# Kernel tuning notes

Measured on AMD Instinct MI355X. Metric: run time of the kernel, lower is better.

The kernel has to match this reference:

```python
import jax, jax.numpy as jnp
import numpy as np

NEG_SLOPE = 0.2

def gat_layer(x, src, dst, W, a_src, a_dst, num_nodes):
    """PyG-style GATConv. W:[F_in,H*C], a_src/a_dst:[H,C]. Returns [N,H,C]."""
    H, C = a_src.shape
    h = (x @ W).reshape(num_nodes, H, C)                      # [N,H,C]
    e_src = jnp.sum(h * a_src, axis=-1)                       # [N,H]
    e_dst = jnp.sum(h * a_dst, axis=-1)                       # [N,H]
    e = jax.nn.leaky_relu(e_src[src] + e_dst[dst], NEG_SLOPE) # [E,H]
    # segment softmax over incoming edges of each destination node
    m = jax.ops.segment_max(e, dst, num_segments=num_nodes)
    w = jnp.exp(e - m[dst])
    z = jax.ops.segment_sum(w, dst, num_segments=num_nodes)
    alpha = w / (z[dst] + 1e-16)                               # [E,H]
    msg = h[src] * alpha[:, :, None]                           # [E,H,C]
    return jax.ops.segment_sum(msg, dst, num_segments=num_nodes)


def setup_inputs() -> dict:
    key = jax.random.key(0)
    ks = jax.random.split(key, 16)
    N, E, F_IN, HID, A, G = 50000, 800000, 128, 128, 32, 64
    x = jax.random.normal(ks[0], (N, F_IN), dtype=jnp.float32)
    edge_index = jax.random.randint(ks[1], (2, E), 0, N, dtype=jnp.int32)
    batch = jnp.sort(jax.random.randint(ks[2], (N,), 0, G, dtype=jnp.int32))
    s = 0.1
    W1 = jax.random.normal(ks[3], (F_IN, 2 * HID), jnp.float32) * s
    a_src1 = jax.random.normal(ks[4], (2, HID), jnp.float32) * s
    a_dst1 = jax.random.normal(ks[5], (2, HID), jnp.float32) * s
    b1 = jnp.zeros((2 * HID,), jnp.float32)
    W2 = jax.random.normal(ks[6], (2 * HID, HID), jnp.float32) * s
    a_src2 = jax.random.normal(ks[7], (1, HID), jnp.float32) * s
    a_dst2 = jax.random.normal(ks[8], (1, HID), jnp.float32) * s
    b2 = jnp.zeros((HID,), jnp.float32)
    Wp = jax.random.normal(ks[9], (HID, A), jnp.float32) * s
    bp = jnp.zeros((A,), jnp.float32)
    Wv = jax.random.normal(ks[10], (HID, 1), jnp.float32) * s
    bv = jnp.zeros((1,), jnp.float32)
    return {"x": x, "edge_index": edge_index, "batch": batch,
            "W1": W1, "a_src1": a_src1, "a_dst1": a_dst1, "b1": b1,
            "W2": W2, "a_src2": a_src2, "a_dst2": a_dst2, "b2": b2,
            "Wp": Wp, "bp": bp, "Wv": Wv, "bv": bv}


def reference(x, edge_index, batch, W1, a_src1, a_dst1, b1,
              W2, a_src2, a_dst2, b2, Wp, bp, Wv, bv):
    N = x.shape[0]
    G = 64  # number of graphs in the batch
    # add self-loops (PyG GATConv default)
    loop = jnp.arange(N, dtype=edge_index.dtype)
    src = jnp.concatenate([edge_index[0], loop])
    dst = jnp.concatenate([edge_index[1], loop])
    # layer 1: heads=2, concat=True
    h1 = gat_layer(x, src, dst, W1, a_src1, a_dst1, N)        # [N,2,HID]
    h1 = jax.nn.elu(h1.reshape(N, -1) + b1)                   # [N,2*HID]
    # layer 2: heads=1, concat=False (mean over heads = identity for H=1)
    h2 = gat_layer(h1, src, dst, W2, a_src2, a_dst2, N)       # [N,1,HID]
    h2 = jax.nn.elu(h2.reshape(N, -1) + b2)                   # [N,HID]
    # global mean pool over graphs
    sums = jax.ops.segment_sum(h2, batch, num_segments=G)
    cnt = jax.ops.segment_sum(jnp.ones((N,), h2.dtype), batch, num_segments=G)
    x_pool = sums / jnp.maximum(cnt, 1.0)[:, None]            # [G,HID]
    policy_logits = x_pool @ Wp + bp                          # [G,A]
    state_value = x_pool @ Wv + bv                            # [G,1]
    return (policy_logits, state_value)
```

## Files before the change

kernel.cpp:

```cpp
#include <hip/hip_runtime.h>
#include <hip/hip_bf16.h>
#include <cstdint>


typedef __attribute__((ext_vector_type(8))) short bf16x8;
typedef __attribute__((ext_vector_type(4))) float f32x4;

#define NBLK_H 160

__device__ __forceinline__ float wave_sum(float v) {
#pragma unroll
    for (int off = 32; off >= 1; off >>= 1) v += __shfl_xor(v, off, 64);
    return v;
}

__device__ __forceinline__ unsigned short f2bf(float f) {
    union { float f; uint32_t u; } c; c.f = f;
    uint32_t u = c.u;
    return (unsigned short)((u + 0x7fffu + ((u >> 16) & 1u)) >> 16);
}

__device__ __forceinline__ float bf2f(unsigned short u) {
    union { uint32_t u; float f; } c; c.u = ((uint32_t)u) << 16;
    return c.f;
}


template <int K, int FOUT>
__device__ __forceinline__ void swizzle_body(const float* __restrict__ W, int ldW, int colOff,
                                             unsigned short* __restrict__ Bsw, int tid) {
    constexpr int CPW = FOUT / 4, NCT = CPW / 16, KST = K / 32;
    if (tid >= K * FOUT / 8) return;
    int lane = tid & 63;
    int rest = tid >> 6;
    int t = rest % KST; rest /= KST;
    int c = rest % NCT; rest /= NCT;
    int cg_ = rest;
    int quad = lane >> 4, lo = lane & 15;
    int col = colOff + cg_ * CPW + c * 16 + lo;
    unsigned short v[8];
#pragma unroll
    for (int j = 0; j < 8; ++j)
        v[j] = f2bf(W[(t * 32 + quad * 8 + j) * ldW + col]);
    ushort4* dst = (ushort4*)(Bsw + (size_t)tid * 8);
    ushort4 o0, o1;
    o0.x = v[0]; o0.y = v[1]; o0.z = v[2]; o0.w = v[3];
    o1.x = v[4]; o1.y = v[5]; o1.z = v[6]; o1.w = v[7];
    dst[0] = o0; dst[1] = o1;
}


__global__ void init_kernel(const float* __restrict__ W1, const float* __restrict__ W2,
                            const float* __restrict__ a_src1, const float* __restrict__ a_dst1,
                            unsigned short* __restrict__ B1h0, unsigned short* __restrict__ B1h1,
                            unsigned short* __restrict__ B2,
                            float* __restrict__ v1s, float* __restrict__ v1d,
                            int* __restrict__ zbase, int zn4) {
    int b = blockIdx.x;
    if (b < 8)        swizzle_body<128, 128>(W1, 256, 0,   B1h0, b * 256 + threadIdx.x);
    else if (b < 16)  swizzle_body<128, 128>(W1, 256, 128, B1h1, (b - 8) * 256 + threadIdx.x);
    else if (b < 32)  swizzle_body<256, 128>(W2, 128, 0,   B2, (b - 16) * 256 + threadIdx.x);
    else if (b == 32) {
        int t = threadIdx.x, h = t >> 7, k = t & 127;
        float vs = 0.f, vd = 0.f;
        for (int c = 0; c < 128; ++c) {
            float w = W1[k * 256 + h * 128 + c];
            vs += w * a_src1[h * 128 + c];
            vd += w * a_dst1[h * 128 + c];
        }
        v1s[h * 128 + k] = vs;
        v1d[h * 128 + k] = vd;
    } else {
        int i = (b - 33) * 256 + threadIdx.x;
        if (i < zn4) ((int4*)zbase)[i] = make_int4(0, 0, 0, 0);
    }
}


__global__ __launch_bounds__(256) void hist_kernel(const int* __restrict__ ei,
                                                   int* __restrict__ hist,
                                                   int E, int ET, int CHUNK, int NB) {
    __shared__ int bins[512];
    const int blk = blockIdx.x;
    for (int t = threadIdx.x; t < NB; t += 256) bins[t] = 0;
    __syncthreads();
    const int start = blk * CHUNK, end = min(ET, start + CHUNK);
    for (int i = start + threadIdx.x; i < end; i += 256) {
        int dst = (i < E) ? ei[E + i] : (i - E);
        atomicAdd(&bins[dst >> 7], 1);
    }
    __syncthreads();
    for (int t = threadIdx.x; t < NB; t += 256) hist[t * NBLK_H + blk] = bins[t];
}

__global__ __launch_bounds__(256) void scan_tiles(int* __restrict__ deg,
                                                  int* __restrict__ tsum, int N) {
    __shared__ int buf[256];
    const int t = threadIdx.x;
    const int base = blockIdx.x * 1024 + t * 4;
    int v[4]; int s = 0;
#pragma unroll
    for (int k = 0; k < 4; ++k) { v[k] = (base + k < N) ? deg[base + k] : 0; s += v[k]; }
    buf[t] = s;
    __syncthreads();
#pragma unroll
    for (int off = 1; off < 256; off <<= 1) {
        int x = (t >= off) ? buf[t - off] : 0;
        __syncthreads();
        buf[t] += x;
        __syncthreads();
    }
    int run = buf[t] - s;
#pragma unroll
    for (int k = 0; k < 4; ++k) {
        if (base + k < N) deg[base + k] = run;
        run += v[k];
    }
    if (t == 255) tsum[blockIdx.x] = buf[255];
}

__global__ __launch_bounds__(256) void scan_add(const int* __restrict__ partial,
                                                const int* __restrict__ tsum,
                                                int* __restrict__ rowptr, int N, int T) {
    __shared__ int s_toff;
    const int tile = blockIdx.x;
    if (threadIdx.x < 64) {
        int t = threadIdx.x;
        int v = (t < T) ? tsum[t] : 0;
#pragma unroll
        for (int off = 1; off < 64; off <<= 1) {
            int x = __shfl_up(v, off, 64);
            if (t >= off) v += x;
        }
        int toff = (tile == 0) ? 0 : __shfl(v, tile - 1, 64);
        if (t == 0) s_toff = toff;
        if (tile == 0 && t == 63) rowptr[N] = v;
    }
    __syncthreads();
    const int toff = s_toff;
    int i = tile * 1024 + threadIdx.x * 4;
#pragma unroll
    for (int k = 0; k < 4; ++k) {
        if (i + k < N) rowptr[i + k] = partial[i + k] + toff;
    }
}

__global__ __launch_bounds__(256) void part_kernel(const int* __restrict__ ei,
                                                   const int* __restrict__ histscan,
                                                   int* __restrict__ bsorted,
                                                   int E, int ET, int CHUNK, int NB) {
    __shared__ int scur[512];
    const int blk = blockIdx.x;
    for (int t = threadIdx.x; t < NB; t += 256) scur[t] = histscan[t * NBLK_H + blk];
    __syncthreads();
    const int start = blk * CHUNK, end = min(ET, start + CHUNK);
    for (int i = start + threadIdx.x; i < end; i += 256) {
        int dst = (i < E) ? ei[E + i] : (i - E);
        int src = (i < E) ? ei[i] : dst;
        int pos = atomicAdd(&scur[dst >> 7], 1);
        bsorted[pos] = (src << 7) | (dst & 127);
    }
}

__global__ __launch_bounds__(256) void bucket_kernel(const int* __restrict__ bsorted,
                                                     const int* __restrict__ histscan,
                                                     int* __restrict__ csr_src,
                                                     int* __restrict__ rowptr,
                                                     int ET, int N, int NB) {
    __shared__ int cnt[128];
    __shared__ int excl[128];
    __shared__ int ebuf[4608];
    const int b = blockIdx.x;
    const int gbase = histscan[b * NBLK_H];
    const int gend  = histscan[(b + 1) * NBLK_H];
    const int sz = gend - gbase;
    const int t = threadIdx.x;
    if (t < 128) cnt[t] = 0;
    __syncthreads();
    const bool fits = (sz <= 4608);
    if (fits) {
        for (int i = t; i < sz; i += 256) {
            int p = bsorted[gbase + i];
            ebuf[i] = p;
            atomicAdd(&cnt[p & 127], 1);
        }
    } else {
        for (int i = t; i < sz; i += 256) {
            int p = bsorted[gbase + i];
            atomicAdd(&cnt[p & 127], 1);
        }
    }
    __syncthreads();
    if (t < 128) excl[t] = cnt[t];
    __syncthreads();
    for (int off = 1; off < 128; off <<= 1) {
        int v = (t < 128 && t >= off) ? excl[t - off] : 0;
        __syncthreads();
        if (t < 128) excl[t] += v;
        __syncthreads();
    }
    if (t < 128) {
        int dst = (b << 7) + t;
        if (dst <= N) rowptr[dst] = gbase + excl[t] - cnt[t];
    }
    __syncthreads();
    if (t < 128) cnt[t] = excl[t] - cnt[t];
    __syncthreads();
    if (fits) {
        for (int i = t; i < sz; i += 256) {
            int p = ebuf[i];
            int pos = atomicAdd(&cnt[p & 127], 1);
            csr_src[gbase + pos] = p >> 7;
        }
    } else {
        for (int i = t; i < sz; i += 256) {
            int p = bsorted[gbase + i];
            int pos = atomicAdd(&cnt[p & 127], 1);
            csr_src[gbase + pos] = p >> 7;
        }
    }
}


__global__ void attn1_cast(const float* __restrict__ x, const float* __restrict__ v1s,
                           const float* __restrict__ v1d, float* __restrict__ es1,
                           float* __restrict__ ed1, unsigned short* __restrict__ xbf, int N) {
    int wid = (blockIdx.x * blockDim.x + threadIdx.x) >> 6;
    int lane = threadIdx.x & 63;
    if (wid >= N) return;
    float2 xv = *(const float2*)(x + (size_t)wid * 128 + lane * 2);
    float p0s = xv.x * v1s[lane * 2] + xv.y * v1s[lane * 2 + 1];
    float p1s = xv.x * v1s[128 + lane * 2] + xv.y * v1s[128 + lane * 2 + 1];
    float p0d = xv.x * v1d[lane * 2] + xv.y * v1d[lane * 2 + 1];
    float p1d = xv.x * v1d[128 + lane * 2] + xv.y * v1d[128 + lane * 2 + 1];
    p0s = wave_sum(p0s); p1s = wave_sum(p1s);
    p0d = wave_sum(p0d); p1d = wave_sum(p1d);
    if (lane == 0) {
        es1[wid * 2] = p0s; es1[wid * 2 + 1] = p1s;
        ed1[wid * 2] = p0d; ed1[wid * 2 + 1] = p1d;
    }
    ushort2 o; o.x = f2bf(xv.x); o.y = f2bf(xv.y);
    *(ushort2*)(xbf + (size_t)wid * 128 + lane * 2) = o;
}


#define ACC2(U_, WW_, P_, Q_) { float v_;                              \
    v_ = bf2f(U_.x); P_.x += WW_.x * v_; Q_.x += WW_.y * v_;           \
    v_ = bf2f(U_.y); P_.y += WW_.x * v_; Q_.y += WW_.y * v_;           \
    v_ = bf2f(U_.z); P_.z += WW_.x * v_; Q_.z += WW_.y * v_;           \
    v_ = bf2f(U_.w); P_.w += WW_.x * v_; Q_.w += WW_.y * v_; }

__global__ void gat_agg_x(const unsigned short* __restrict__ xbf,
                          const float* __restrict__ es, const float* __restrict__ ed,
                          const int* __restrict__ rowptr, const int* __restrict__ csr_src,
                          unsigned short* __restrict__ aggx, int N, int NPAD) {
    __shared__ float2 w_lds[4][32];
    __shared__ int    s_lds[4][32];
    int wid = (blockIdx.x * blockDim.x + threadIdx.x) >> 6;
    int lane = threadIdx.x & 63;
    if (wid >= N) return;
    const int wave = threadIdx.x >> 6;
    const int rs = rowptr[wid], re = rowptr[wid + 1];
    const int half = lane >> 5, c = lane & 31;
    const float edn = ed[wid * 2 + half];

    float z = 0.f;
    float4 p0 = {0.f, 0.f, 0.f, 0.f}, p1 = {0.f, 0.f, 0.f, 0.f};
    float4 q0 = {0.f, 0.f, 0.f, 0.f}, q1 = {0.f, 0.f, 0.f, 0.f};
    for (int i = rs; i < re; i += 32) {
        const int cnt = min(re - i, 32);
        if (c < cnt) {
            int s = csr_src[i + c];
            float e = es[s * 2 + half] + edn;
            e = (e > 0.f) ? e : 0.2f * e;
            float ww = __expf(e);
            ((float*)&w_lds[wave][c])[half] = ww;
            if (half == 0) s_lds[wave][c] = s;
            z += ww;
        }
        int k = half;
        for (; k + 6 < cnt; k += 8) {
            int s0 = s_lds[wave][k + 0], s1 = s_lds[wave][k + 2];
            int s2 = s_lds[wave][k + 4], s3 = s_lds[wave][k + 6];
            float2 wv0 = w_lds[wave][k + 0], wv1 = w_lds[wave][k + 2];
            float2 wv2 = w_lds[wave][k + 4], wv3 = w_lds[wave][k + 6];
            ushort4 u0 = *(const ushort4*)(xbf + (size_t)s0 * 128 + c * 4);
            ushort4 u1 = *(const ushort4*)(xbf + (size_t)s1 * 128 + c * 4);
            ushort4 u2 = *(const ushort4*)(xbf + (size_t)s2 * 128 + c * 4);
            ushort4 u3 = *(const ushort4*)(xbf + (size_t)s3 * 128 + c * 4);
            ACC2(u0, wv0, p0, q0);
            ACC2(u1, wv1, p1, q1);
            ACC2(u2, wv2, p0, q0);
            ACC2(u3, wv3, p1, q1);
        }
        for (; k < cnt; k += 2) {
            int s0 = s_lds[wave][k];
            float2 wv = w_lds[wave][k];
            ushort4 u0 = *(const ushort4*)(xbf + (size_t)s0 * 128 + c * 4);
            ACC2(u0, wv, p0, q0);
        }
    }
#pragma unroll
    for (int off = 16; off >= 1; off >>= 1) z += __shfl_xor(z, off, 64);
    const float rz = 1.f / (z + 1e-16f);
    float4 p, q;
    p.x = p0.x + p1.x; p.y = p0.y + p1.y; p.z = p0.z + p1.z; p.w = p0.w + p1.w;
    q.x = q0.x + q1.x; q.y = q0.y + q1.y; q.z = q0.z + q1.z; q.w = q0.w + q1.w;
    p.x += __shfl_xor(p.x, 32, 64); p.y += __shfl_xor(p.y, 32, 64);
    p.z += __shfl_xor(p.z, 32, 64); p.w += __shfl_xor(p.w, 32, 64);
    q.x += __shfl_xor(q.x, 32, 64); q.y += __shfl_xor(q.y, 32, 64);
    q.z += __shfl_xor(q.z, 32, 64); q.w += __shfl_xor(q.w, 32, 64);
    float ox = (half ? q.x : p.x) * rz;
    float oy = (half ? q.y : p.y) * rz;
    float oz = (half ? q.z : p.z) * rz;
    float ow = (half ? q.w : p.w) * rz;
    ushort4 o;
    o.x = f2bf(ox); o.y = f2bf(oy); o.z = f2bf(oz); o.w = f2bf(ow);
    *(ushort4*)(aggx + ((size_t)half * NPAD + wid) * 128 + c * 4) = o;
}


__global__ __launch_bounds__(256) void gemm_plain(const unsigned short* __restrict__ Abase,
                                                  const unsigned short* __restrict__ B0,
                                                  const unsigned short* __restrict__ B1sw,
                                                  const float* __restrict__ bias,
                                                  unsigned short* __restrict__ C,
                                                  int N, int NPAD) {
    constexpr int K = 128, FOUT = 128;
    constexpr int CPW = FOUT / 4, NCT = CPW / 16, KST = K / 32;
    const int head = blockIdx.y;
    const unsigned short* A = Abase + (size_t)head * NPAD * 128;
    const unsigned short* Bsw = head ? B1sw : B0;
    const int colOff = head * 128;
    const int tid = threadIdx.x;
    const int wave = tid >> 6, lane = tid & 63;
    const int quad = lane >> 4, lo = lane & 15;
    const int n0 = blockIdx.x * 64;
    const int c0 = wave * CPW;

    bf16x8 bf[NCT][KST];
    {
        const bf16x8* Bp = (const bf16x8*)Bsw;
#pragma unroll
        for (int c = 0; c < NCT; ++c)
#pragma unroll
            for (int t = 0; t < KST; ++t)
                bf[c][t] = Bp[((wave * NCT + c) * KST + t) * 64 + lane];
    }

    f32x4 acc[4][NCT];
#pragma unroll
    for (int r = 0; r < 4; ++r)
#pragma unroll
        for (int c = 0; c < NCT; ++c) acc[r][c] = (f32x4){0.f, 0.f, 0.f, 0.f};

#pragma unroll
    for (int r = 0; r < 4; ++r) {
        const unsigned short* Ar = A + (size_t)(n0 + r * 16 + lo) * K + quad * 8;
#pragma unroll
        for (int t = 0; t < KST; ++t) {
            bf16x8 af = *(const bf16x8*)(Ar + t * 32);
#pragma unroll
            for (int c = 0; c < NCT; ++c)
                acc[r][c] = __builtin_amdgcn_mfma_f32_16x16x32_bf16(af, bf[c][t], acc[r][c],
                                                                   0, 0, 0);
        }
    }

#pragma unroll
    for (int r = 0; r < 4; ++r) {
        int row = n0 + r * 16 + quad * 4;
#pragma unroll
        for (int c = 0; c < NCT; ++c) {
            int col = colOff + c0 + c * 16 + lo;
            float bv = bias[col];
#pragma unroll
            for (int j = 0; j < 4; ++j) {
                if (row + j < N) {
                    float v = acc[r][c][j] + bv;
                    v = (v > 0.f) ? v : __expf(v) - 1.f;
                    C[(size_t)(row + j) * 256 + col] = f2bf(v);
                }
            }
        }
    }
}


__global__ __launch_bounds__(256) void gemm2_kernel(const unsigned short* __restrict__ A,
                                                    const unsigned short* __restrict__ Bsw,
                                                    const float* __restrict__ a_src,
                                                    const float* __restrict__ a_dst,
                                                    float* __restrict__ es, float* __restrict__ ed,
                                                    unsigned short* __restrict__ C, int N) {
    constexpr int K = 256, FOUT = 128;
    constexpr int CPW = FOUT / 4, NCT = CPW / 16, KST = K / 32;
    const int tid = threadIdx.x;
    const int wave = tid >> 6, lane = tid & 63;
    const int quad = lane >> 4, lo = lane & 15;
    const int n0 = blockIdx.x * 64;
    const int c0 = wave * CPW;
    __shared__ float lds_ps[4][64];
    __shared__ float lds_pd[4][64];

    bf16x8 bf[NCT][KST];
    {
        const bf16x8* Bp = (const bf16x8*)Bsw;
#pragma unroll
        for (int c = 0; c < NCT; ++c)
#pragma unroll
            for (int t = 0; t < KST; ++t)
                bf[c][t] = Bp[((wave * NCT + c) * KST + t) * 64 + lane];
    }

    f32x4 acc[4][NCT];
#pragma unroll
    for (int r = 0; r < 4; ++r)
#pragma unroll
        for (int c = 0; c < NCT; ++c) acc[r][c] = (f32x4){0.f, 0.f, 0.f, 0.f};

#pragma unroll
    for (int r = 0; r < 4; ++r) {
        const unsigned short* Ar = A + (size_t)(n0 + r * 16 + lo) * K + quad * 8;
#pragma unroll
        for (int t = 0; t < KST; ++t) {
            bf16x8 af = *(const bf16x8*)(Ar + t * 32);
#pragma unroll
            for (int c = 0; c < NCT; ++c)
                acc[r][c] = __builtin_amdgcn_mfma_f32_16x16x32_bf16(af, bf[c][t], acc[r][c],
                                                                   0, 0, 0);
        }
    }

#pragma unroll
    for (int r = 0; r < 4; ++r) {
        int row = n0 + r * 16 + quad * 4;
#pragma unroll
        for (int c = 0; c < NCT; ++c) {
            int col = c0 + c * 16 + lo;
#pragma unroll
            for (int j = 0; j < 4; ++j)
                if (row + j < N) C[(size_t)(row + j) * FOUT + col] = f2bf(acc[r][c][j]);
        }
    }

    float asv[NCT], adv[NCT];
#pragma unroll
    for (int c = 0; c < NCT; ++c) {
        int col = c0 + c * 16 + lo;
        asv[c] = a_src[col];
        adv[c] = a_dst[col];
    }
#pragma unroll
    for (int r = 0; r < 4; ++r) {
#pragma unroll
        for (int j = 0; j < 4; ++j) {
            float ps = 0.f, pd = 0.f;
#pragma unroll
            for (int c = 0; c < NCT; ++c) { ps += acc[r][c][j] * asv[c]; pd += acc[r][c][j] * adv[c]; }
#pragma unroll
            for (int off = 1; off <= 8; off <<= 1) {
                ps += __shfl_xor(ps, off, 64);
                pd += __shfl_xor(pd, off, 64);
            }
            if (lo == 0) {
                int row_l = r * 16 + quad * 4 + j;
                lds_ps[wave][row_l] = ps;
                lds_pd[wave][row_l] = pd;
            }
        }
    }
    __syncthreads();
    if (tid < 64) {
        int row = tid;
        int n = n0 + row;
        if (n < N) {
            es[n] = lds_ps[0][row] + lds_ps[1][row] + lds_ps[2][row] + lds_ps[3][row];
            ed[n] = lds_pd[0][row] + lds_pd[1][row] + lds_pd[2][row] + lds_pd[3][row];
        }
    }
}


__global__ void gat_agg_h1(const unsigned short* __restrict__ Hpre,
                           const float* __restrict__ es, const float* __restrict__ ed,
                           const int* __restrict__ rowptr, const int* __restrict__ csr_src,
                           const float* __restrict__ bias, unsigned short* __restrict__ out,
                           int N) {
    __shared__ float w_lds[4][64];
    __shared__ int   s_lds[4][64];
    int wid = (blockIdx.x * blockDim.x + threadIdx.x) >> 6;
    int lane = threadIdx.x & 63;
    if (wid >= N) return;
    const int wave = threadIdx.x >> 6;
    const int rs = rowptr[wid], re = rowptr[wid + 1];
    const int half = lane >> 5, c = lane & 31;
    const float edn = ed[wid];

    float z = 0.f;
    float4 a0 = {0.f, 0.f, 0.f, 0.f}, a1 = {0.f, 0.f, 0.f, 0.f};
    float4 a2 = {0.f, 0.f, 0.f, 0.f}, a3 = {0.f, 0.f, 0.f, 0.f};
    for (int i = rs; i < re; i += 64) {
        const int cnt = min(re - i, 64);
        if (lane < cnt) {
            int s = csr_src[i + lane];
            float e = es[s] + edn;
            e = (e > 0.f) ? e : 0.2f * e;
            float ww = __expf(e);
            w_lds[wave][lane] = ww;
            s_lds[wave][lane] = s;
            z += ww;
        }
        int k = half;
        for (; k + 14 < cnt; k += 16) {
            int s0 = s_lds[wave][k],      s1 = s_lds[wave][k + 2];
            int s2 = s_lds[wave][k + 4],  s3 = s_lds[wave][k + 6];
            int s4 = s_lds[wave][k + 8],  s5 = s_lds[wave][k + 10];
            int s6 = s_lds[wave][k + 12], s7 = s_lds[wave][k + 14];
            float w0 = w_lds[wave][k],      w1 = w_lds[wave][k + 2];
            float w2 = w_lds[wave][k + 4],  w3 = w_lds[wave][k + 6];
            float w4 = w_lds[wave][k + 8],  w5 = w_lds[wave][k + 10];
            float w6 = w_lds[wave][k + 12], w7 = w_lds[wave][k + 14];
            ushort4 u0 = *(const ushort4*)(Hpre + (size_t)s0 * 128 + c * 4);
            ushort4 u1 = *(const ushort4*)(Hpre + (size_t)s1 * 128 + c * 4);
            ushort4 u2 = *(const ushort4*)(Hpre + (size_t)s2 * 128 + c * 4);
            ushort4 u3 = *(const ushort4*)(Hpre + (size_t)s3 * 128 + c * 4);
            ushort4 u4 = *(const ushort4*)(Hpre + (size_t)s4 * 128 + c * 4);
            ushort4 u5 = *(const ushort4*)(Hpre + (size_t)s5 * 128 + c * 4);
            ushort4 u6 = *(const ushort4*)(Hpre + (size_t)s6 * 128 + c * 4);
            ushort4 u7 = *(const ushort4*)(Hpre + (size_t)s7 * 128 + c * 4);
            a0.x += w0 * bf2f(u0.x); a0.y += w0 * bf2f(u0.y);
            a0.z += w0 * bf2f(u0.z); a0.w += w0 * bf2f(u0.w);
            a1.x += w1 * bf2f(u1.x); a1.y += w1 * bf2f(u1.y);
            a1.z += w1 * bf2f(u1.z); a1.w += w1 * bf2f(u1.w);
            a2.x += w2 * bf2f(u2.x); a2.y += w2 * bf2f(u2.y);
            a2.z += w2 * bf2f(u2.z); a2.w += w2 * bf2f(u2.w);
            a3.x += w3 * bf2f(u3.x); a3.y += w3 * bf2f(u3.y);
            a3.z += w3 * bf2f(u3.z); a3.w += w3 * bf2f(u3.w);
            a0.x += w4 * bf2f(u4.x); a0.y += w4 * bf2f(u4.y);
            a0.z += w4 * bf2f(u4.z); a0.w += w4 * bf2f(u4.w);
            a1.x += w5 * bf2f(u5.x); a1.y += w5 * bf2f(u5.y);
            a1.z += w5 * bf2f(u5.z); a1.w += w5 * bf2f(u5.w);
            a2.x += w6 * bf2f(u6.x); a2.y += w6 * bf2f(u6.y);
            a2.z += w6 * bf2f(u6.z); a2.w += w6 * bf2f(u6.w);
            a3.x += w7 * bf2f(u7.x); a3.y += w7 * bf2f(u7.y);
            a3.z += w7 * bf2f(u7.z); a3.w += w7 * bf2f(u7.w);
        }
        for (; k + 6 < cnt; k += 8) {
            int s0 = s_lds[wave][k], s1 = s_lds[wave][k + 2];
            int s2 = s_lds[wave][k + 4], s3 = s_lds[wave][k + 6];
            float w0 = w_lds[wave][k], w1 = w_lds[wave][k + 2];
            float w2 = w_lds[wave][k + 4], w3 = w_lds[wave][k + 6];
            ushort4 u0 = *(const ushort4*)(Hpre + (size_t)s0 * 128 + c * 4);
            ushort4 u1 = *(const ushort4*)(Hpre + (size_t)s1 * 128 + c * 4);
            ushort4 u2 = *(const ushort4*)(Hpre + (size_t)s2 * 128 + c * 4);
            ushort4 u3 = *(const ushort4*)(Hpre + (size_t)s3 * 128 + c * 4);
            a0.x += w0 * bf2f(u0.x); a0.y += w0 * bf2f(u0.y);
            a0.z += w0 * bf2f(u0.z); a0.w += w0 * bf2f(u0.w);
            a1.x += w1 * bf2f(u1.x); a1.y += w1 * bf2f(u1.y);
            a1.z += w1 * bf2f(u1.z); a1.w += w1 * bf2f(u1.w);
            a2.x += w2 * bf2f(u2.x); a2.y += w2 * bf2f(u2.y);
            a2.z += w2 * bf2f(u2.z); a2.w += w2 * bf2f(u2.w);
            a3.x += w3 * bf2f(u3.x); a3.y += w3 * bf2f(u3.y);
            a3.z += w3 * bf2f(u3.z); a3.w += w3 * bf2f(u3.w);
        }
        for (; k < cnt; k += 2) {
            int s0 = s_lds[wave][k];
            float w0 = w_lds[wave][k];
            ushort4 u0 = *(const ushort4*)(Hpre + (size_t)s0 * 128 + c * 4);
            a0.x += w0 * bf2f(u0.x); a0.y += w0 * bf2f(u0.y);
            a0.z += w0 * bf2f(u0.z); a0.w += w0 * bf2f(u0.w);
        }
    }
    z = wave_sum(z);
    const float rz = 1.f / (z + 1e-16f);

    float ox = a0.x + a1.x + a2.x + a3.x;
    float oy = a0.y + a1.y + a2.y + a3.y;
    float oz = a0.z + a1.z + a2.z + a3.z;
    float ow = a0.w + a1.w + a2.w + a3.w;
    ox += __shfl_xor(ox, 32, 64);
    oy += __shfl_xor(oy, 32, 64);
    oz += __shfl_xor(oz, 32, 64);
    ow += __shfl_xor(ow, 32, 64);
    if (lane < 32) {
        float4 bv = ((const float4*)bias)[c];
        ox = ox * rz + bv.x; oy = oy * rz + bv.y; oz = oz * rz + bv.z; ow = ow * rz + bv.w;
        ox = (ox > 0.f) ? ox : __expf(ox) - 1.f;
        oy = (oy > 0.f) ? oy : __expf(oy) - 1.f;
        oz = (oz > 0.f) ? oz : __expf(oz) - 1.f;
        ow = (ow > 0.f) ? ow : __expf(ow) - 1.f;
        ushort4 o;
        o.x = f2bf(ox); o.y = f2bf(oy); o.z = f2bf(oz); o.w = f2bf(ow);
        *(ushort4*)(out + (size_t)wid * 128 + c * 4) = o;
    }
}


#define PCHUNK 256

__global__ __launch_bounds__(256) void pool_partial(const unsigned short* __restrict__ h2,
                                                    const int* __restrict__ batch,
                                                    float* __restrict__ xsum,
                                                    int* __restrict__ cnt, int N) {
    const int base = blockIdx.x * PCHUNK;
    const int rg = threadIdx.x >> 6;
    const int c2 = threadIdx.x & 63;
    float ax = 0.f, ay = 0.f;
    int gcur = -1, run = 0;
    for (int r = rg; r < PCHUNK; r += 4) {
        int i = base + r;
        if (i >= N) break;
        int g = batch[i];
        if (g != gcur) {
            if (gcur >= 0) {
                atomicAdd(&xsum[gcur * 128 + c2 * 2 + 0], ax);
                atomicAdd(&xsum[gcur * 128 + c2 * 2 + 1], ay);
                if (c2 == 0) atomicAdd(&cnt[gcur], run);
            }
            gcur = g; ax = 0.f; ay = 0.f; run = 0;
        }
        ushort2 u = *(const ushort2*)(h2 + (size_t)i * 128 + c2 * 2);
        ax += bf2f(u.x); ay += bf2f(u.y);
        run += 1;
    }
    if (gcur >= 0) {
        atomicAdd(&xsum[gcur * 128 + c2 * 2 + 0], ax);
        atomicAdd(&xsum[gcur * 128 + c2 * 2 + 1], ay);
        if (c2 == 0) atomicAdd(&cnt[gcur], run);
    }
}


__global__ void head_kernel(const float* __restrict__ xsum, const int* __restrict__ cnt,
                            const float* __restrict__ Wp, const float* __restrict__ bp,
                            const float* __restrict__ Wv, const float* __restrict__ bv,
                            float* __restrict__ out) {
    int g = blockIdx.x, t = threadIdx.x;
    __shared__ float p[128];
    float inv = 1.f / fmaxf((float)cnt[g], 1.f);
    p[t] = xsum[g * 128 + t] * inv;
    p[t + 64] = xsum[g * 128 + t + 64] * inv;
    __syncthreads();
    if (t < 32) {
        float acc = bp[t];
        for (int k = 0; k < 128; ++k) acc += p[k] * Wp[k * 32 + t];
        out[g * 32 + t] = acc;
    } else if (t == 32) {
        float acc = bv[0];
        for (int k = 0; k < 128; ++k) acc += p[k] * Wv[k];
        out[64 * 32 + g] = acc;
    }
}


extern "C" void kernel_launch(void* const* d_in, const int* in_sizes, int n_in,
                              void* d_out, int out_size, void* d_ws, size_t ws_size,
                              hipStream_t stream) {
    const float* x      = (const float*)d_in[0];
    const int*   ei     = (const int*)d_in[1];
    const int*   batch  = (const int*)d_in[2];
    const float* W1     = (const float*)d_in[3];
    const float* a_src1 = (const float*)d_in[4];
    const float* a_dst1 = (const float*)d_in[5];
    const float* b1     = (const float*)d_in[6];
    const float* W2     = (const float*)d_in[7];
    const float* a_src2 = (const float*)d_in[8];
    const float* a_dst2 = (const float*)d_in[9];
    const float* b2     = (const float*)d_in[10];
    const float* Wp     = (const float*)d_in[11];
    const float* bp     = (const float*)d_in[12];
    const float* Wv     = (const float*)d_in[13];
    const float* bv     = (const float*)d_in[14];

    const int N  = in_sizes[0] / 128;
    const int E  = in_sizes[1] / 2;
    const int ET = E + N;
    const int NPAD = ((N + 63) / 64) * 64;
    const int NBLK = NPAD / 64;
    const int PBLK = (N + PCHUNK - 1) / PCHUNK;
    const int NB = (N + 127) >> 7;
    const int CHUNK = (ET + NBLK_H - 1) / NBLK_H;
    const int M = NB * NBLK_H;
    const int TILESH = (M + 1023) / 1024;

    char* ws = (char*)d_ws;
    size_t off = 0;
    auto alloc = [&](size_t bytes) -> void* {
        void* p = ws + off;
        off = (off + bytes + 255) & ~(size_t)255;
        return p;
    };
    unsigned short* xbf   = (unsigned short*)alloc((size_t)NPAD * 128 * 2);
    unsigned short* aggx  = (unsigned short*)alloc((size_t)2 * NPAD * 128 * 2);
    unsigned short* h1bf  = (unsigned short*)alloc((size_t)NPAD * 256 * 2);
    unsigned short* h2pre = (unsigned short*)alloc((size_t)NPAD * 128 * 2);
    unsigned short* h2bf  = (unsigned short*)alloc((size_t)N * 128 * 2);
    unsigned short* w1h0  = (unsigned short*)alloc((size_t)128 * 128 * 2);
    unsigned short* w1h1  = (unsigned short*)alloc((size_t)128 * 128 * 2);
    unsigned short* w2sw  = (unsigned short*)alloc((size_t)256 * 128 * 2);
    float* v1s = (float*)alloc(256 * 4);
    float* v1d = (float*)alloc(256 * 4);
    float* es1 = (float*)alloc((size_t)N * 2 * 4);
    float* ed1 = (float*)alloc((size_t)N * 2 * 4);
    float* es2 = (float*)alloc((size_t)N * 4);
    float* ed2 = (float*)alloc((size_t)N * 4);
    const int ZINTS = 64 * 128 + 64;
    int*   zbase  = (int*)alloc(((size_t)ZINTS + 8) * 4);
    float* xsum   = (float*)zbase;
    int*   cnt    = (int*)(xsum + 64 * 128);
    int*   rowptr   = (int*)alloc((size_t)(N + 1) * 4);
    int*   hist     = (int*)alloc((size_t)M * 4);
    int*   histscan = (int*)alloc((size_t)(M + 1) * 4);
    int*   bsorted  = (int*)alloc((size_t)ET * 4);
    int*   csrsrc   = (int*)alloc((size_t)ET * 4);
    int*   tsum     = (int*)alloc(64 * 4);
    const int zn4 = (ZINTS + 3) / 4;

    init_kernel<<<33 + (zn4 + 255) / 256, 256, 0, stream>>>(W1, W2, a_src1, a_dst1,
                                                            w1h0, w1h1, w2sw, v1s, v1d,
                                                            zbase, zn4);

    hist_kernel<<<NBLK_H, 256, 0, stream>>>(ei, hist, E, ET, CHUNK, NB);
    scan_tiles<<<TILESH, 256, 0, stream>>>(hist, tsum, M);
    scan_add<<<TILESH, 256, 0, stream>>>(hist, tsum, histscan, M, TILESH);
    part_kernel<<<NBLK_H, 256, 0, stream>>>(ei, histscan, bsorted, E, ET, CHUNK, NB);
    bucket_kernel<<<NB, 256, 0, stream>>>(bsorted, histscan, csrsrc, rowptr, ET, N, NB);

    attn1_cast<<<(N + 3) / 4, 256, 0, stream>>>(x, v1s, v1d, es1, ed1, xbf, N);
    gat_agg_x<<<(N + 3) / 4, 256, 0, stream>>>(xbf, es1, ed1, rowptr, csrsrc, aggx, N, NPAD);
    gemm_plain<<<dim3(NBLK, 2), 256, 0, stream>>>(aggx, w1h0, w1h1, b1, h1bf, N, NPAD);

    gemm2_kernel<<<NBLK, 256, 0, stream>>>(h1bf, w2sw, a_src2, a_dst2, es2, ed2, h2pre, N);
    gat_agg_h1<<<(N + 3) / 4, 256, 0, stream>>>(h2pre, es2, ed2, rowptr, csrsrc, b2,
                                                h2bf, N);

    pool_partial<<<PBLK, 256, 0, stream>>>(h2bf, batch, xsum, cnt, N);
    head_kernel<<<64, 64, 0, stream>>>(xsum, cnt, Wp, bp, Wv, bv, (float*)d_out);
}
```

Baseline: 319.0 us.

## Fuse GEMM1+GEMM2 via LDS, merge setup kernels, shrink CSR buckets

Fuses the layer-1 GEMM (with bias and ELU) and the layer-2 GEMM into one kernel that keeps the h1 tile in LDS, so the h1 round trip through global memory goes away. The histogram is folded into init_kernel, and the tile scan is merged with attn1_cast into one launch. CSR buckets shrink from 128 to 64 nodes, with a larger scan, and the x aggregation loop is unrolled 16-wide. This cuts launch count and memory traffic but raises LDS use in the fused GEMM, which may lower occupancy.

```diff
diff --git a/kernel.cpp b/kernel.cpp
--- a/kernel.cpp
+++ b/kernel.cpp
@@ -7,6 +7,8 @@
 typedef __attribute__((ext_vector_type(4))) float f32x4;
 
 #define NBLK_H 160
+#define BSH 6
+#define BMSK 63
 
 __device__ __forceinline__ float wave_sum(float v) {
 #pragma unroll
@@ -50,12 +52,16 @@
 }
 
 
-__global__ void init_kernel(const float* __restrict__ W1, const float* __restrict__ W2,
-                            const float* __restrict__ a_src1, const float* __restrict__ a_dst1,
-                            unsigned short* __restrict__ B1h0, unsigned short* __restrict__ B1h1,
-                            unsigned short* __restrict__ B2,
-                            float* __restrict__ v1s, float* __restrict__ v1d,
-                            int* __restrict__ zbase, int zn4) {
+__global__ __launch_bounds__(256) void init_kernel(
+        const float* __restrict__ W1, const float* __restrict__ W2,
+        const float* __restrict__ a_src1, const float* __restrict__ a_dst1,
+        unsigned short* __restrict__ B1h0, unsigned short* __restrict__ B1h1,
+        unsigned short* __restrict__ B2,
+        float* __restrict__ v1s, float* __restrict__ v1d,
+        int* __restrict__ zbase, int zn4, int ZB,
+        const int* __restrict__ ei, int* __restrict__ hist,
+        int E, int ET, int CHUNK, int NB) {
+    __shared__ int bins[1024];
     int b = blockIdx.x;
     if (b < 8)        swizzle_body<128, 128>(W1, 256, 0,   B1h0, b * 256 + threadIdx.x);
     else if (b < 16)  swizzle_body<128, 128>(W1, 256, 128, B1h1, (b - 8) * 256 + threadIdx.x);
@@ -70,162 +76,56 @@
         }
         v1s[h * 128 + k] = vs;
         v1d[h * 128 + k] = vd;
-    } else {
+    } else if (b < 33 + ZB) {
         int i = (b - 33) * 256 + threadIdx.x;
         if (i < zn4) ((int4*)zbase)[i] = make_int4(0, 0, 0, 0);
-    }
-}
-
-
-__global__ __launch_bounds__(256) void hist_kernel(const int* __restrict__ ei,
-                                                   int* __restrict__ hist,
-                                                   int E, int ET, int CHUNK, int NB) {
-    __shared__ int bins[512];
-    const int blk = blockIdx.x;
-    for (int t = threadIdx.x; t < NB; t += 256) bins[t] = 0;
-    __syncthreads();
-    const int start = blk * CHUNK, end = min(ET, start + CHUNK);
-    for (int i = start + threadIdx.x; i < end; i += 256) {
-        int dst = (i < E) ? ei[E + i] : (i - E);
-        atomicAdd(&bins[dst >> 7], 1);
-    }
-    __syncthreads();
-    for (int t = threadIdx.x; t < NB; t += 256) hist[t * NBLK_H + blk] = bins[t];
-}
-
-__global__ __launch_bounds__(256) void scan_tiles(int* __restrict__ deg,
-                                                  int* __restrict__ tsum, int N) {
+    } else {
+        const int blk = b - 33 - ZB;
+        for (int t = threadIdx.x; t < NB; t += 256) bins[t] = 0;
+        __syncthreads();
+        const int start = blk * CHUNK, end = min(ET, start + CHUNK);
+        for (int i = start + threadIdx.x; i < end; i += 256) {
+            int dst = (i < E) ? ei[E + i] : (i - E);
+            atomicAdd(&bins[dst >> BSH], 1);
+        }
+        __syncthreads();
+        for (int t = threadIdx.x; t < NB; t += 256) hist[t * NBLK_H + blk] = bins[t];
+    }
+}
+
+
+__global__ __launch_bounds__(256) void scan_attn1(
+        int* __restrict__ hist, int* __restrict__ tsum, int M, int TILESH,
+        const float* __restrict__ x, const float* __restrict__ v1s,
+        const float* __restrict__ v1d, float* __restrict__ es1,
+        float* __restrict__ ed1, unsigned short* __restrict__ xbf, int N) {
     __shared__ int buf[256];
-    const int t = threadIdx.x;
-    const int base = blockIdx.x * 1024 + t * 4;
-    int v[4]; int s = 0;
-#pragma unroll
-    for (int k = 0; k < 4; ++k) { v[k] = (base + k < N) ? deg[base + k] : 0; s += v[k]; }
-    buf[t] = s;
-    __syncthreads();
-#pragma unroll
-    for (int off = 1; off < 256; off <<= 1) {
-        int x = (t >= off) ? buf[t - off] : 0;
+    if ((int)blockIdx.x < TILESH) {
+        const int t = threadIdx.x;
+        const int base = blockIdx.x * 1024 + t * 4;
+        int v[4]; int s = 0;
+#pragma unroll
+        for (int k = 0; k < 4; ++k) { v[k] = (base + k < M) ? hist[base + k] : 0; s += v[k]; }
+        buf[t] = s;
         __syncthreads();
-        buf[t] += x;
-        __syncthreads();
-    }
-    int run = buf[t] - s;
-#pragma unroll
-    for (int k = 0; k < 4; ++k) {
-        if (base + k < N) deg[base + k] = run;
-        run += v[k];
-    }
-    if (t == 255) tsum[blockIdx.x] = buf[255];
-}
-
-__global__ __launch_bounds__(256) void scan_add(const int* __restrict__ partial,
-                                                const int* __restrict__ tsum,
-                                                int* __restrict__ rowptr, int N, int T) {
-    __shared__ int s_toff;
-    const int tile = blockIdx.x;
-    if (threadIdx.x < 64) {
-        int t = threadIdx.x;
-        int v = (t < T) ? tsum[t] : 0;
-#pragma unroll
-        for (int off = 1; off < 64; off <<= 1) {
-            int x = __shfl_up(v, off, 64);
-            if (t >= off) v += x;
-        }
-        int toff = (tile == 0) ? 0 : __shfl(v, tile - 1, 64);
-        if (t == 0) s_toff = toff;
-        if (tile == 0 && t == 63) rowptr[N] = v;
-    }
-    __syncthreads();
-    const int toff = s_toff;
-    int i = tile * 1024 + threadIdx.x * 4;
-#pragma unroll
-    for (int k = 0; k < 4; ++k) {
-        if (i + k < N) rowptr[i + k] = partial[i + k] + toff;
-    }
-}
-
-__global__ __launch_bounds__(256) void part_kernel(const int* __restrict__ ei,
-                                                   const int* __restrict__ histscan,
-                                                   int* __restrict__ bsorted,
-                                                   int E, int ET, int CHUNK, int NB) {
-    __shared__ int scur[512];
-    const int blk = blockIdx.x;
-    for (int t = threadIdx.x; t < NB; t += 256) scur[t] = histscan[t * NBLK_H + blk];
-    __syncthreads();
-    const int start = blk * CHUNK, end = min(ET, start + CHUNK);
-    for (int i = start + threadIdx.x; i < end; i += 256) {
-        int dst = (i < E) ? ei[E + i] : (i - E);
-        int src = (i < E) ? ei[i] : dst;
-        int pos = atomicAdd(&scur[dst >> 7], 1);
-        bsorted[pos] = (src << 7) | (dst & 127);
-    }
-}
-
-__global__ __launch_bounds__(256) void bucket_kernel(const int* __restrict__ bsorted,
-                                                     const int* __restrict__ histscan,
-                                                     int* __restrict__ csr_src,
-                                                     int* __restrict__ rowptr,
-                                                     int ET, int N, int NB) {
-    __shared__ int cnt[128];
-    __shared__ int excl[128];
-    __shared__ int ebuf[4608];
-    const int b = blockIdx.x;
-    const int gbase = histscan[b * NBLK_H];
-    const int gend  = histscan[(b + 1) * NBLK_H];
-    const int sz = gend - gbase;
-    const int t = threadIdx.x;
-    if (t < 128) cnt[t] = 0;
-    __syncthreads();
-    const bool fits = (sz <= 4608);
-    if (fits) {
-        for (int i = t; i < sz; i += 256) {
-            int p = bsorted[gbase + i];
-            ebuf[i] = p;
-            atomicAdd(&cnt[p & 127], 1);
-        }
-    } else {
-        for (int i = t; i < sz; i += 256) {
-            int p = bsorted[gbase + i];
-            atomicAdd(&cnt[p & 127], 1);
-        }
-    }
-    __syncthreads();
-    if (t < 128) excl[t] = cnt[t];
-    __syncthreads();
-    for (int off = 1; off < 128; off <<= 1) {
-        int v = (t < 128 && t >= off) ? excl[t - off] : 0;
-        __syncthreads();
-        if (t < 128) excl[t] += v;
-        __syncthreads();
-    }
-    if (t < 128) {
-        int dst = (b << 7) + t;
-        if (dst <= N) rowptr[dst] = gbase + excl[t] - cnt[t];
-    }
-    __syncthreads();
-    if (t < 128) cnt[t] = excl[t] - cnt[t];
-    __syncthreads();
-    if (fits) {
-        for (int i = t; i < sz; i += 256) {
-            int p = ebuf[i];
-            int pos = atomicAdd(&cnt[p & 127], 1);
-            csr_src[gbase + pos] = p >> 7;
-        }
-    } else {
-        for (int i = t; i < sz; i += 256) {
-            int p = bsorted[gbase + i];
-            int pos = atomicAdd(&cnt[p & 127], 1);
-            csr_src[gbase + pos] = p >> 7;
-        }
-    }
-}
-
-
-__global__ void attn1_cast(const float* __restrict__ x, const float* __restrict__ v1s,
-                           const float* __restrict__ v1d, float* __restrict__ es1,
-                           float* __restrict__ ed1, unsigned short* __restrict__ xbf, int N) {
-    int wid = (blockIdx.x * blockDim.x + threadIdx.x) >> 6;
+#pragma unroll
+        for (int off = 1; off < 256; off <<= 1) {
+            int xx = (t >= off) ? buf[t - off] : 0;
+            __syncthreads();
+            buf[t] += xx;
+            __syncthreads();
+        }
+        int run = buf[t] - s;
+#pragma unroll
+        for (int k = 0; k < 4; ++k) {
+            if (base + k < M) hist[base + k] = run;
+            run += v[k];
+        }
+        if (t == 255) tsum[blockIdx.x] = buf[255];
+        return;
+    }
+    int bid = blockIdx.x - TILESH;
+    int wid = (bid * 256 + threadIdx.x) >> 6;
     int lane = threadIdx.x & 63;
     if (wid >= N) return;
     float2 xv = *(const float2*)(x + (size_t)wid * 128 + lane * 2);
@@ -241,6 +141,107 @@
     }
     ushort2 o; o.x = f2bf(xv.x); o.y = f2bf(xv.y);
     *(ushort2*)(xbf + (size_t)wid * 128 + lane * 2) = o;
+}
+
+__global__ __launch_bounds__(256) void scan_add(const int* __restrict__ partial,
+                                                const int* __restrict__ tsum,
+                                                int* __restrict__ out, int M, int T) {
+    __shared__ int sb[256];
+    const int t = threadIdx.x;
+    sb[t] = (t < T) ? tsum[t] : 0;
+    __syncthreads();
+#pragma unroll
+    for (int off = 1; off < 256; off <<= 1) {
+        int v = (t >= off) ? sb[t - off] : 0;
+        __syncthreads();
+        sb[t] += v;
+        __syncthreads();
+    }
+    const int tile = blockIdx.x;
+    if (tile == 0 && t == 0) out[M] = sb[255];
+    const int toff = (tile == 0) ? 0 : sb[tile - 1];
+    int i = tile * 1024 + t * 4;
+#pragma unroll
+    for (int k = 0; k < 4; ++k) {
+        if (i + k < M) out[i + k] = partial[i + k] + toff;
+    }
+}
+
+__global__ __launch_bounds__(256) void part_kernel(const int* __restrict__ ei,
+                                                   const int* __restrict__ histscan,
+                                                   int* __restrict__ bsorted,
+                                                   int E, int ET, int CHUNK, int NB) {
+    __shared__ int scur[1024];
+    const int blk = blockIdx.x;
+    for (int t = threadIdx.x; t < NB; t += 256) scur[t] = histscan[t * NBLK_H + blk];
+    __syncthreads();
+    const int start = blk * CHUNK, end = min(ET, start + CHUNK);
+    for (int i = start + threadIdx.x; i < end; i += 256) {
+        int dst = (i < E) ? ei[E + i] : (i - E);
+        int src = (i < E) ? ei[i] : dst;
+        int pos = atomicAdd(&scur[dst >> BSH], 1);
+        bsorted[pos] = (src << BSH) | (dst & BMSK);
+    }
+}
+
+__global__ __launch_bounds__(256) void bucket_kernel(const int* __restrict__ bsorted,
+                                                     const int* __restrict__ histscan,
+                                                     int* __restrict__ csr_src,
+                                                     int* __restrict__ rowptr,
+                                                     int N, int NB) {
+    __shared__ int cnt[64];
+    __shared__ int excl[64];
+    __shared__ int ebuf[2304];
+    const int b = blockIdx.x;
+    const int gbase = histscan[b * NBLK_H];
+    const int gend  = histscan[(b + 1) * NBLK_H];
+    const int sz = gend - gbase;
+    const int t = threadIdx.x;
+    if (b == 0 && t == 255) rowptr[N] = histscan[NB * NBLK_H];
+    if (t < 64) cnt[t] = 0;
+    __syncthreads();
+    const bool fits = (sz <= 2304);
+    if (fits) {
+        for (int i = t; i < sz; i += 256) {
+            int p = bsorted[gbase + i];
+            ebuf[i] = p;
+            atomicAdd(&cnt[p & BMSK], 1);
+        }
+    } else {
+        for (int i = t; i < sz; i += 256) {
+            int p = bsorted[gbase + i];
+            atomicAdd(&cnt[p & BMSK], 1);
+        }
+    }
+    __syncthreads();
+    if (t < 64) excl[t] = cnt[t];
+    __syncthreads();
+    for (int off = 1; off < 64; off <<= 1) {
+        int v = (t < 64 && t >= off) ? excl[t - off] : 0;
+        __syncthreads();
+        if (t < 64) excl[t] += v;
+        __syncthreads();
+    }
+    if (t < 64) {
+        int dst = (b << BSH) + t;
+        if (dst < N) rowptr[dst] = gbase + excl[t] - cnt[t];
+    }
+    __syncthreads();
+    if (t < 64) cnt[t] = excl[t] - cnt[t];
+    __syncthreads();
+    if (fits) {
+        for (int i = t; i < sz; i += 256) {
+            int p = ebuf[i];
+            int pos = atomicAdd(&cnt[p & BMSK], 1);
+            csr_src[gbase + pos] = p >> BSH;
+        }
+    } else {
+        for (int i = t; i < sz; i += 256) {
+            int p = bsorted[gbase + i];
+            int pos = atomicAdd(&cnt[p & BMSK], 1);
+            csr_src[gbase + pos] = p >> BSH;
+        }
+    }
 }
 
 
@@ -279,6 +280,32 @@
             z += ww;
         }
         int k = half;
+        for (; k + 14 < cnt; k += 16) {
+            int s0 = s_lds[wave][k + 0],  s1 = s_lds[wave][k + 2];
+            int s2 = s_lds[wave][k + 4],  s3 = s_lds[wave][k + 6];
+            int s4 = s_lds[wave][k + 8],  s5 = s_lds[wave][k + 10];
+            int s6 = s_lds[wave][k + 12], s7 = s_lds[wave][k + 14];
+            float2 wv0 = w_lds[wave][k + 0],  wv1 = w_lds[wave][k + 2];
+            float2 wv2 = w_lds[wave][k + 4],  wv3 = w_lds[wave][k + 6];
+            float2 wv4 = w_lds[wave][k + 8],  wv5 = w_lds[wave][k + 10];
+            float2 wv6 = w_lds[wave][k + 12], wv7 = w_lds[wave][k + 14];
+            ushort4 u0 = *(const ushort4*)(xbf + (size_t)s0 * 128 + c * 4);
+            ushort4 u1 = *(const ushort4*)(xbf + (size_t)s1 * 128 + c * 4);
+            ushort4 u2 = *(const ushort4*)(xbf + (size_t)s2 * 128 + c * 4);
+            ushort4 u3 = *(const ushort4*)(xbf + (size_t)s3 * 128 + c * 4);
+            ushort4 u4 = *(const ushort4*)(xbf + (size_t)s4 * 128 + c * 4);
+            ushort4 u5 = *(const ushort4*)(xbf + (size_t)s5 * 128 + c * 4);
+            ushort4 u6 = *(const ushort4*)(xbf + (size_t)s6 * 128 + c * 4);
+            ushort4 u7 = *(const ushort4*)(xbf + (size_t)s7 * 128 + c * 4);
+            ACC2(u0, wv0, p0, q0);
+            ACC2(u1, wv1, p1, q1);
+            ACC2(u2, wv2, p0, q0);
+            ACC2(u3, wv3, p1, q1);
+            ACC2(u4, wv4, p0, q0);
+            ACC2(u5, wv5, p1, q1);
+            ACC2(u6, wv6, p0, q0);
+            ACC2(u7, wv7, p1, q1);
+        }
         for (; k + 6 < cnt; k += 8) {
             int s0 = s_lds[wave][k + 0], s1 = s_lds[wave][k + 2];
             int s2 = s_lds[wave][k + 4], s3 = s_lds[wave][k + 6];
@@ -320,133 +347,108 @@
 }
 
 
-__global__ __launch_bounds__(256) void gemm_plain(const unsigned short* __restrict__ Abase,
-                                                  const unsigned short* __restrict__ B0,
-                                                  const unsigned short* __restrict__ B1sw,
-                                                  const float* __restrict__ bias,
-                                                  unsigned short* __restrict__ C,
-                                                  int N, int NPAD) {
-    constexpr int K = 128, FOUT = 128;
-    constexpr int CPW = FOUT / 4, NCT = CPW / 16, KST = K / 32;
-    const int head = blockIdx.y;
-    const unsigned short* A = Abase + (size_t)head * NPAD * 128;
-    const unsigned short* Bsw = head ? B1sw : B0;
-    const int colOff = head * 128;
+__global__ __launch_bounds__(256) void gemm12_fused(
+        const unsigned short* __restrict__ Abase,
+        const unsigned short* __restrict__ B1h0, const unsigned short* __restrict__ B1h1,
+        const unsigned short* __restrict__ B2sw,
+        const float* __restrict__ b1,
+        const float* __restrict__ a_src, const float* __restrict__ a_dst,
+        float* __restrict__ es, float* __restrict__ ed,
+        unsigned short* __restrict__ C, int N, int NPAD) {
+    __shared__ unsigned short h1t[64][264];
+    __shared__ float lds_ps[4][64];
+    __shared__ float lds_pd[4][64];
     const int tid = threadIdx.x;
     const int wave = tid >> 6, lane = tid & 63;
     const int quad = lane >> 4, lo = lane & 15;
     const int n0 = blockIdx.x * 64;
-    const int c0 = wave * CPW;
-
-    bf16x8 bf[NCT][KST];
+
     {
-        const bf16x8* Bp = (const bf16x8*)Bsw;
-#pragma unroll
-        for (int c = 0; c < NCT; ++c)
-#pragma unroll
-            for (int t = 0; t < KST; ++t)
-                bf[c][t] = Bp[((wave * NCT + c) * KST + t) * 64 + lane];
-    }
-
-    f32x4 acc[4][NCT];
+        const int head = wave >> 1, wh = wave & 1;
+        const unsigned short* A = Abase + (size_t)head * NPAD * 128;
+        const bf16x8* Bp = (const bf16x8*)(head ? B1h1 : B1h0);
+        bf16x8 bf[4][4];
+#pragma unroll
+        for (int c = 0; c < 4; ++c)
+#pragma unroll
+            for (int t = 0; t < 4; ++t)
+                bf[c][t] = Bp[((wh * 4 + c) * 4 + t) * 64 + lane];
+        f32x4 acc[4][4];
+#pragma unroll
+        for (int r = 0; r < 4; ++r)
+#pragma unroll
+            for (int c = 0; c < 4; ++c) acc[r][c] = (f32x4){0.f, 0.f, 0.f, 0.f};
+#pragma unroll
+        for (int r = 0; r < 4; ++r) {
+            const unsigned short* Ar = A + (size_t)(n0 + r * 16 + lo) * 128 + quad * 8;
+#pragma unroll
+            for (int t = 0; t < 4; ++t) {
+                bf16x8 af = *(const bf16x8*)(Ar + t * 32);
+#pragma unroll
+                for (int c = 0; c < 4; ++c)
+                    acc[r][c] = __builtin_amdgcn_mfma_f32_16x16x32_bf16(af, bf[c][t],
+                                                                       acc[r][c], 0, 0, 0);
+            }
+        }
+#pragma unroll
+        for (int r = 0; r < 4; ++r) {
+            int rl = r * 16 + quad * 4;
+#pragma unroll
+            for (int c = 0; c < 4; ++c) {
+                int col = head * 128 + wh * 64 + c * 16 + lo;
+                float bv = b1[col];
+#pragma unroll
+                for (int j = 0; j < 4; ++j) {
+                    float v = acc[r][c][j] + bv;
+                    v = (v > 0.f) ? v : __expf(v) - 1.f;
+                    h1t[rl + j][col] = f2bf(v);
+                }
+            }
+        }
+    }
+    __syncthreads();
+
+    bf16x8 bf2[2][8];
+    {
+        const bf16x8* Bp2 = (const bf16x8*)B2sw;
+#pragma unroll
+        for (int c = 0; c < 2; ++c)
+#pragma unroll
+            for (int t = 0; t < 8; ++t)
+                bf2[c][t] = Bp2[((wave * 2 + c) * 8 + t) * 64 + lane];
+    }
+    f32x4 acc2[4][2];
 #pragma unroll
     for (int r = 0; r < 4; ++r)
 #pragma unroll
-        for (int c = 0; c < NCT; ++c) acc[r][c] = (f32x4){0.f, 0.f, 0.f, 0.f};
-
+        for (int c = 0; c < 2; ++c) acc2[r][c] = (f32x4){0.f, 0.f, 0.f, 0.f};
 #pragma unroll
     for (int r = 0; r < 4; ++r) {
-        const unsigned short* Ar = A + (size_t)(n0 + r * 16 + lo) * K + quad * 8;
-#pragma unroll
-        for (int t = 0; t < KST; ++t) {
+        const unsigned short* Ar = &h1t[r * 16 + lo][quad * 8];
+#pragma unroll
+        for (int t = 0; t < 8; ++t) {
             bf16x8 af = *(const bf16x8*)(Ar + t * 32);
 #pragma unroll
-            for (int c = 0; c < NCT; ++c)
-                acc[r][c] = __builtin_amdgcn_mfma_f32_16x16x32_bf16(af, bf[c][t], acc[r][c],
-                                                                   0, 0, 0);
-        }
-    }
-
+            for (int c = 0; c < 2; ++c)
+                acc2[r][c] = __builtin_amdgcn_mfma_f32_16x16x32_bf16(af, bf2[c][t],
+                                                                    acc2[r][c], 0, 0, 0);
+        }
+    }
+    const int c0 = wave * 32;
 #pragma unroll
     for (int r = 0; r < 4; ++r) {
         int row = n0 + r * 16 + quad * 4;
 #pragma unroll
-        for (int c = 0; c < NCT; ++c) {
-            int col = colOff + c0 + c * 16 + lo;
-            float bv = bias[col];
-#pragma unroll
-            for (int j = 0; j < 4; ++j) {
-                if (row + j < N) {
-                    float v = acc[r][c][j] + bv;
-                    v = (v > 0.f) ? v : __expf(v) - 1.f;
-                    C[(size_t)(row + j) * 256 + col] = f2bf(v);
-                }
-            }
-        }
-    }
-}
-
-
-__global__ __launch_bounds__(256) void gemm2_kernel(const unsigned short* __restrict__ A,
-                                                    const unsigned short* __restrict__ Bsw,
-                                                    const float* __restrict__ a_src,
-                                                    const float* __restrict__ a_dst,
-                                                    float* __restrict__ es, float* __restrict__ ed,
-                                                    unsigned short* __restrict__ C, int N) {
-    constexpr int K = 256, FOUT = 128;
-    constexpr int CPW = FOUT / 4, NCT = CPW / 16, KST = K / 32;
-    const int tid = threadIdx.x;
-    const int wave = tid >> 6, lane = tid & 63;
-    const int quad = lane >> 4, lo = lane & 15;
-    const int n0 = blockIdx.x * 64;
-    const int c0 = wave * CPW;
-    __shared__ float lds_ps[4][64];
-    __shared__ float lds_pd[4][64];
-
-    bf16x8 bf[NCT][KST];
-    {
-        const bf16x8* Bp = (const bf16x8*)Bsw;
-#pragma unroll
-        for (int c = 0; c < NCT; ++c)
-#pragma unroll
-            for (int t = 0; t < KST; ++t)
-                bf[c][t] = Bp[((wave * NCT + c) * KST + t) * 64 + lane];
-    }
-
-    f32x4 acc[4][NCT];
-#pragma unroll
-    for (int r = 0; r < 4; ++r)
-#pragma unroll
-        for (int c = 0; c < NCT; ++c) acc[r][c] = (f32x4){0.f, 0.f, 0.f, 0.f};
-
-#pragma unroll
-    for (int r = 0; r < 4; ++r) {
-        const unsigned short* Ar = A + (size_t)(n0 + r * 16 + lo) * K + quad * 8;
-#pragma unroll
-        for (int t = 0; t < KST; ++t) {
-            bf16x8 af = *(const bf16x8*)(Ar + t * 32);
-#pragma unroll
-            for (int c = 0; c < NCT; ++c)
-                acc[r][c] = __builtin_amdgcn_mfma_f32_16x16x32_bf16(af, bf[c][t], acc[r][c],
-                                                                   0, 0, 0);
-        }
-    }
-
-#pragma unroll
-    for (int r = 0; r < 4; ++r) {
-        int row = n0 + r * 16 + quad * 4;
-#pragma unroll
-        for (int c = 0; c < NCT; ++c) {
+        for (int c = 0; c < 2; ++c) {
             int col = c0 + c * 16 + lo;
 #pragma unroll
             for (int j = 0; j < 4; ++j)
-                if (row + j < N) C[(size_t)(row + j) * FOUT + col] = f2bf(acc[r][c][j]);
-        }
-    }
-
-    float asv[NCT], adv[NCT];
-#pragma unroll
-    for (int c = 0; c < NCT; ++c) {
+                if (row + j < N) C[(size_t)(row + j) * 128 + col] = f2bf(acc2[r][c][j]);
+        }
+    }
+    float asv[2], adv[2];
+#pragma unroll
+    for (int c = 0; c < 2; ++c) {
         int col = c0 + c * 16 + lo;
         asv[c] = a_src[col];
         adv[c] = a_dst[col];
@@ -457,7 +459,7 @@
         for (int j = 0; j < 4; ++j) {
             float ps = 0.f, pd = 0.f;
 #pragma unroll
-            for (int c = 0; c < NCT; ++c) { ps += acc[r][c][j] * asv[c]; pd += acc[r][c][j] * adv[c]; }
+            for (int c = 0; c < 2; ++c) { ps += acc2[r][c][j] * asv[c]; pd += acc2[r][c][j] * adv[c]; }
 #pragma unroll
             for (int off = 1; off <= 8; off <<= 1) {
                 ps += __shfl_xor(ps, off, 64);
@@ -679,10 +681,11 @@
     const int NPAD = ((N + 63) / 64) * 64;
     const int NBLK = NPAD / 64;
     const int PBLK = (N + PCHUNK - 1) / PCHUNK;
-    const int NB = (N + 127) >> 7;
+    const int NB = (N + 63) >> BSH;
     const int CHUNK = (ET + NBLK_H - 1) / NBLK_H;
     const int M = NB * NBLK_H;
     const int TILESH = (M + 1023) / 1024;
+    const int AB = (N + 3) / 4;
 
     char* ws = (char*)d_ws;
     size_t off = 0;
@@ -693,7 +696,6 @@
     };
     unsigned short* xbf   = (unsigned short*)alloc((size_t)NPAD * 128 * 2);
     unsigned short* aggx  = (unsigned short*)alloc((size_t)2 * NPAD * 128 * 2);
-    unsigned short* h1bf  = (unsigned short*)alloc((size_t)NPAD * 256 * 2);
     unsigned short* h2pre = (unsigned short*)alloc((size_t)NPAD * 128 * 2);
     unsigned short* h2bf  = (unsigned short*)alloc((size_t)N * 128 * 2);
     unsigned short* w1h0  = (unsigned short*)alloc((size_t)128 * 128 * 2);
@@ -714,27 +716,24 @@
     int*   histscan = (int*)alloc((size_t)(M + 1) * 4);
     int*   bsorted  = (int*)alloc((size_t)ET * 4);
     int*   csrsrc   = (int*)alloc((size_t)ET * 4);
-    int*   tsum     = (int*)alloc(64 * 4);
+    int*   tsum     = (int*)alloc(256 * 4);
     const int zn4 = (ZINTS + 3) / 4;
-
-    init_kernel<<<33 + (zn4 + 255) / 256, 256, 0, stream>>>(W1, W2, a_src1, a_dst1,
-                                                            w1h0, w1h1, w2sw, v1s, v1d,
-                                                            zbase, zn4);
-
-    hist_kernel<<<NBLK_H, 256, 0, stream>>>(ei, hist, E, ET, CHUNK, NB);
-    scan_tiles<<<TILESH, 256, 0, stream>>>(hist, tsum, M);
+    const int ZB = (zn4 + 255) / 256;
+
+    init_kernel<<<33 + ZB + NBLK_H, 256, 0, stream>>>(W1, W2, a_src1, a_dst1,
+                                                      w1h0, w1h1, w2sw, v1s, v1d,
+                                                      zbase, zn4, ZB,
+                                                      ei, hist, E, ET, CHUNK, NB);
+    scan_attn1<<<TILESH + AB, 256, 0, stream>>>(hist, tsum, M, TILESH,
+                                                x, v1s, v1d, es1, ed1, xbf, N);
     scan_add<<<TILESH, 256, 0, stream>>>(hist, tsum, histscan, M, TILESH);
     part_kernel<<<NBLK_H, 256, 0, stream>>>(ei, histscan, bsorted, E, ET, CHUNK, NB);
-    bucket_kernel<<<NB, 256, 0, stream>>>(bsorted, histscan, csrsrc, rowptr, ET, N, NB);
-
-    attn1_cast<<<(N + 3) / 4, 256, 0, stream>>>(x, v1s, v1d, es1, ed1, xbf, N);
+    bucket_kernel<<<NB, 256, 0, stream>>>(bsorted, histscan, csrsrc, rowptr, N, NB);
     gat_agg_x<<<(N + 3) / 4, 256, 0, stream>>>(xbf, es1, ed1, rowptr, csrsrc, aggx, N, NPAD);
-    gemm_plain<<<dim3(NBLK, 2), 256, 0, stream>>>(aggx, w1h0, w1h1, b1, h1bf, N, NPAD);
-
-    gemm2_kernel<<<NBLK, 256, 0, stream>>>(h1bf, w2sw, a_src2, a_dst2, es2, ed2, h2pre, N);
+    gemm12_fused<<<NBLK, 256, 0, stream>>>(aggx, w1h0, w1h1, w2sw, b1,
+                                           a_src2, a_dst2, es2, ed2, h2pre, N, NPAD);
     gat_agg_h1<<<(N + 3) / 4, 256, 0, stream>>>(h2pre, es2, ed2, rowptr, csrsrc, b2,
                                                 h2bf, N);
-
     pool_partial<<<PBLK, 256, 0, stream>>>(h2bf, batch, xsum, cnt, N);
     head_kernel<<<64, 64, 0, stream>>>(xsum, cnt, Wp, bp, Wv, bv, (float*)d_out);
 }
```

Measured after the change: 291.5 us. 1.09x faster.
